# Optimization experiments

Measured on AMD Instinct MI355X. Metric: run time of the kernel, lower is better.

The kernel has to match this reference:

```python
import jax, jax.numpy as jnp
import numpy as np

DIM = 1024
HEADS = 16
HEAD_DIM = DIM // HEADS
SCALE = 1.0 / float(np.sqrt(HEAD_DIM))


def complex_linear(x, w_r, w_i, b_r, b_i):
    # x: (..., in, 2) with trailing real/imag channel
    xr, xi = x[..., 0], x[..., 1]
    lin_rr = xr @ w_r.T + b_r
    lin_ii = xi @ w_i.T + b_i
    lin_ri = xr @ w_i.T + b_i
    lin_ir = xi @ w_r.T + b_r
    out_r = lin_rr - lin_ii
    out_i = lin_ri + lin_ir
    return jnp.stack([out_r, out_i], axis=-1)


def setup_inputs() -> dict:
    key = jax.random.key(0)
    ks = jax.random.split(key, 9)
    B, N = 2, 2048
    s_in = 1.0 / np.sqrt(DIM)
    inp = {
        "x": jax.random.normal(ks[0], (B, N, DIM, 2), dtype=jnp.float32),
        "wqkv_r": jax.random.uniform(ks[1], (3 * DIM, DIM), jnp.float32, -s_in, s_in),
        "wqkv_i": jax.random.uniform(ks[2], (3 * DIM, DIM), jnp.float32, -s_in, s_in),
        "bqkv_r": jax.random.uniform(ks[3], (3 * DIM,), jnp.float32, -s_in, s_in),
        "bqkv_i": jax.random.uniform(ks[4], (3 * DIM,), jnp.float32, -s_in, s_in),
        "wo_r": jax.random.uniform(ks[5], (DIM, DIM), jnp.float32, -s_in, s_in),
        "wo_i": jax.random.uniform(ks[6], (DIM, DIM), jnp.float32, -s_in, s_in),
        "bo_r": jax.random.uniform(ks[7], (DIM,), jnp.float32, -s_in, s_in),
        "bo_i": jax.random.uniform(ks[8], (DIM,), jnp.float32, -s_in, s_in),
    }
    return inp


def reference(x, wqkv_r, wqkv_i, bqkv_r, bqkv_i, wo_r, wo_i, bo_r, bo_i):
    B, N, C, _ = x.shape
    qkv = complex_linear(x, wqkv_r, wqkv_i, bqkv_r, bqkv_i)  # (B,N,3C,2)
    q, k, v = jnp.split(qkv, 3, axis=-2)
    q = q.reshape(B, N, HEADS, HEAD_DIM, 2)
    k = k.reshape(B, N, HEADS, HEAD_DIM, 2)
    v = v.reshape(B, N, HEADS, HEAD_DIM, 2)
    # contract over head_dim AND complex channel: Re(q . conj(k))
    attn = jnp.einsum('bnhdc,bmhdc->bhnm', q, k) * SCALE
    attn = jax.nn.softmax(attn, axis=-1)
    out = jnp.einsum('bhnm,bmhdc->bnhdc', attn, v).reshape(B, N, C, 2)
    return complex_linear(out, wo_r, wo_i, bo_r, bo_i)
```

## Files before the change

### kernel.cpp

```cpp
#include <hip/hip_runtime.h>

using f16 = _Float16;
typedef f16 f16x8 __attribute__((ext_vector_type(8)));
typedef f16 f16x4 __attribute__((ext_vector_type(4)));
typedef float f32x4 __attribute__((ext_vector_type(4)));

#define TOKENS 4096
#define KD 2048
#define NQ 6144
#define QKW 4128
#define VTS 2064

__device__ __forceinline__ void gload_lds16(const void* g, void* l) {
  __builtin_amdgcn_global_load_lds(
      (__attribute__((address_space(1))) void*)(unsigned long long)g,
      (__attribute__((address_space(3))) void*)l, 16, 0, 0);
}

__global__ __launch_bounds__(256) void cast_x_kernel(const float* __restrict__ x,
                                                     f16* __restrict__ X, int n8) {
  int i = blockIdx.x * 256 + threadIdx.x;
  if (i >= n8) return;
  const float4* p = (const float4*)x + (size_t)i * 2;
  float4 a = p[0], b = p[1];
  f16x8 v = {(f16)a.x, (f16)a.y, (f16)a.z, (f16)a.w,
             (f16)b.x, (f16)b.y, (f16)b.z, (f16)b.w};
  *(f16x8*)(X + (size_t)i * 8) = v;
}

__global__ __launch_bounds__(256) void pack_wqkv_kernel(const float* __restrict__ wr,
    const float* __restrict__ wi, const float* __restrict__ br, const float* __restrict__ bi,
    f16* __restrict__ Wp, float* __restrict__ biasq) {
  int idx = blockIdx.x * 256 + threadIdx.x;
  if (idx >= NQ * 256) return;
  int j = idx >> 8, kc = idx & 255;
  int which = j >> 11, rem = j & 2047;
  int h = rem >> 7, t = rem & 127, d = t >> 1, c = t & 1;
  int o = which * 1024 + h * 64 + d;
  const float4 wr4 = *(const float4*)(wr + (size_t)o * 1024 + kc * 4);
  const float4 wi4 = *(const float4*)(wi + (size_t)o * 1024 + kc * 4);
  f16x8 v;
  const float wrs[4] = {wr4.x, wr4.y, wr4.z, wr4.w};
  const float wis[4] = {wi4.x, wi4.y, wi4.z, wi4.w};
  #pragma unroll
  for (int tt = 0; tt < 4; ++tt) {
    v[2 * tt]     = (f16)((c == 0) ? wrs[tt] : wis[tt]);
    v[2 * tt + 1] = (f16)((c == 0) ? -wis[tt] : wrs[tt]);
  }
  *(f16x8*)(Wp + (size_t)j * KD + kc * 8) = v;
  if (kc == 0) biasq[j] = (c == 0) ? (br[o] - bi[o]) : (br[o] + bi[o]);
}

__global__ __launch_bounds__(256) void pack_wo_kernel(const float* __restrict__ wr,
    const float* __restrict__ wi, const float* __restrict__ br, const float* __restrict__ bi,
    f16* __restrict__ Wp, float* __restrict__ biaso) {
  int idx = blockIdx.x * 256 + threadIdx.x;
  if (idx >= KD * 256) return;
  int j = idx >> 8, kc = idx & 255;
  int jo = j >> 1, c = j & 1;
  const float4 wr4 = *(const float4*)(wr + (size_t)jo * 1024 + kc * 4);
  const float4 wi4 = *(const float4*)(wi + (size_t)jo * 1024 + kc * 4);
  f16x8 v;
  const float wrs[4] = {wr4.x, wr4.y, wr4.z, wr4.w};
  const float wis[4] = {wi4.x, wi4.y, wi4.z, wi4.w};
  #pragma unroll
  for (int tt = 0; tt < 4; ++tt) {
    v[2 * tt]     = (f16)((c == 0) ? wrs[tt] : wis[tt]);
    v[2 * tt + 1] = (f16)((c == 0) ? -wis[tt] : wrs[tt]);
  }
  *(f16x8*)(Wp + (size_t)j * KD + kc * 8) = v;
  if (kc == 0) biaso[j] = (c == 0) ? (br[jo] - bi[jo]) : (br[jo] + bi[jo]);
}

template<bool QKV, int NTN>
__global__ __launch_bounds__(256, 3) void gemm_v5(const f16* __restrict__ A,
    const f16* __restrict__ B, const float* __restrict__ bias,
    f16* __restrict__ qkout, f16* __restrict__ vt, float* __restrict__ fout) {
  __shared__ __align__(16) f16 lA[128 * 64];
  __shared__ __align__(16) f16 lB[128 * 64];

  const int tid = threadIdx.x;
  const int wave = tid >> 6, lane = tid & 63;
  const int lo = lane & 15, hi = lane >> 4;
  const int wm = wave >> 1, wn = wave & 1;

  const int nwg = gridDim.x, cpx = nwg / 8;
  const int bid = blockIdx.x;
  const int wg = (bid & 7) * cpx + (bid >> 3);
  const int tm = wg / NTN, tn = wg % NTN;
  const int m0 = tm * 128, n0 = tn * 128;

  const f16* gA = A + (size_t)m0 * KD;
  const f16* gB = B + (size_t)n0 * KD;

  auto stage = [&](f16* ldsX, const f16* g) {
    #pragma unroll
    for (int is = 0; is < 4; ++is) {
      const int L = is * 256 + tid;
      const int row = L >> 3, cp = L & 7;
      gload_lds16(g + (size_t)row * KD + ((cp ^ (row & 7)) * 8),
                  ldsX + (size_t)(is * 256 + wave * 64) * 8);
    }
  };
  auto readA = [&](f16x8* dst, int kk) {
    #pragma unroll
    for (int i = 0; i < 4; ++i) {
      const int row = wm * 64 + i * 16 + lo;
      const int ch = (kk * 4 + hi) ^ (row & 7);
      dst[i] = *(const f16x8*)&lA[row * 64 + ch * 8];
    }
  };
  auto readB = [&](f16x8* dst, int kk) {
    #pragma unroll
    for (int i = 0; i < 4; ++i) {
      const int row = wn * 64 + i * 16 + lo;
      const int ch = (kk * 4 + hi) ^ (row & 7);
      dst[i] = *(const f16x8*)&lB[row * 64 + ch * 8];
    }
  };

  f32x4 acc[4][4] = {};

  for (int kt = 0; kt < KD; kt += 64) {
    __syncthreads();
    stage(lA, gA + kt);
    stage(lB, gB + kt);
    __syncthreads();
    f16x8 a[4], b[4];
    readA(a, 0); readB(b, 0);
    #pragma unroll
    for (int mi = 0; mi < 4; ++mi)
      #pragma unroll
      for (int ni = 0; ni < 4; ++ni)
        acc[mi][ni] = __builtin_amdgcn_mfma_f32_16x16x32_f16(a[mi], b[ni], acc[mi][ni], 0, 0, 0);
    readA(a, 1); readB(b, 1);
    #pragma unroll
    for (int mi = 0; mi < 4; ++mi)
      #pragma unroll
      for (int ni = 0; ni < 4; ++ni)
        acc[mi][ni] = __builtin_amdgcn_mfma_f32_16x16x32_f16(a[mi], b[ni], acc[mi][ni], 0, 0, 0);
  }

  #pragma unroll
  for (int mi = 0; mi < 4; ++mi) {
    #pragma unroll
    for (int ni = 0; ni < 4; ++ni) {
      const int colbase = n0 + wn * 64 + ni * 16;
      const int col = colbase + lo;
      const float bv = bias[col];
      const int rowb = m0 + wm * 64 + mi * 16 + hi * 4;
      if (QKV && colbase >= 4096) {
        const int dcol = col - 4096;
        const int hh = dcol >> 7, dd = dcol & 127;
        const int bb = rowb >> 11, tok = rowb & 2047;
        f16x4 pk;
        #pragma unroll
        for (int r = 0; r < 4; ++r) pk[r] = (f16)(acc[mi][ni][r] + bv);
        *(f16x4*)(vt + ((size_t)(bb * 16 + hh) * 128 + dd) * VTS + tok) = pk;
      } else if (QKV) {
        #pragma unroll
        for (int r = 0; r < 4; ++r)
          qkout[(size_t)(rowb + r) * QKW + col] = (f16)(acc[mi][ni][r] + bv);
      } else {
        #pragma unroll
        for (int r = 0; r < 4; ++r)
          fout[(size_t)(rowb + r) * KD + col] = acc[mi][ni][r] + bv;
      }
    }
  }
}

__global__ __launch_bounds__(256) void attn_kernel(const f16* __restrict__ qk,
                                                   const f16* __restrict__ vt,
                                                   f16* __restrict__ outp) {
  __shared__ __align__(16) f16 lds[2][8192];
  const int tid = threadIdx.x;
  const int wave = tid >> 6, lane = tid & 63;
  const int lo = lane & 15, hi = lane >> 4;

  const int flat = blockIdx.x;
  const int nf = (flat & 7) * 64 + (flat >> 3);
  const int by = nf >> 4, bx = nf & 15;
  const int b = by >> 4, h = by & 15;
  const int q0 = bx * 128 + wave * 32;

  const f16* Qb = qk + (size_t)b * 2048 * QKW + h * 128;
  const f16* Kb = Qb + 2048;
  const f16* Vtb = vt + (size_t)(b * 16 + h) * 128 * VTS;

  f16x8 qf[2][4];
  #pragma unroll
  for (int qb = 0; qb < 2; ++qb)
    #pragma unroll
    for (int c = 0; c < 4; ++c) {
      qf[qb][c] = *(const f16x8*)(Qb + (size_t)(q0 + qb * 16 + lo) * QKW + c * 32 + hi * 8);
      qf[qb][c] *= (f16)0.125f;
    }

  f32x4 o[2][8];
  #pragma unroll
  for (int qb = 0; qb < 2; ++qb)
    #pragma unroll
    for (int dc = 0; dc < 8; ++dc) o[qb][dc] = (f32x4){0.f, 0.f, 0.f, 0.f};
  float m_run[2] = {-INFINITY, -INFINITY};
  float l_run[2] = {0.f, 0.f};

  const int cl0 = wave * 64 + lane;

  auto STAGE = [&](int buf, int t) {
    #pragma unroll
    for (int rnd = 0; rnd < 2; ++rnd) {
      const int cl = rnd * 256 + cl0;
      const int row = cl >> 4;
      const int gch = (cl & 15) ^ (row & 7);
      gload_lds16(Kb + (size_t)(t + row) * QKW + gch * 8,
                  &lds[buf][(size_t)(rnd * 256 + wave * 64) * 8]);
    }
    #pragma unroll
    for (int rnd = 0; rnd < 2; ++rnd) {
      const int cl = rnd * 256 + cl0;
      const int d = cl >> 2;
      const int gch = (cl & 3) ^ ((d >> 1) & 3);
      gload_lds16(Vtb + (size_t)d * VTS + t + gch * 8,
                  &lds[buf][4096 + (size_t)(rnd * 256 + wave * 64) * 8]);
    }
  };

  STAGE(0, 0);
  int cur = 0;

  for (int it = 0; it < 64; ++it) {
    __syncthreads();
    if (it + 1 < 64) STAGE(cur ^ 1, (it + 1) * 32);

    const f16* ldsK = lds[cur];
    const f16* ldsV = lds[cur] + 4096;

    f16x8 kf[2][4];
    #pragma unroll
    for (int tt = 0; tt < 2; ++tt)
      #pragma unroll
      for (int c = 0; c < 4; ++c) {
        const int row = tt * 16 + lo;
        const int ch = (c * 4 + hi) ^ (row & 7);
        kf[tt][c] = *(const f16x8*)&ldsK[row * 128 + ch * 8];
      }

    f16x4 pf[2][2];
    #pragma unroll
    for (int qb = 0; qb < 2; ++qb) {
      f32x4 s0 = {0.f, 0.f, 0.f, 0.f}, s1 = {0.f, 0.f, 0.f, 0.f};
      #pragma unroll
      for (int c = 0; c < 4; ++c) {
        s0 = __builtin_amdgcn_mfma_f32_16x16x32_f16(kf[0][c], qf[qb][c], s0, 0, 0, 0);
        s1 = __builtin_amdgcn_mfma_f32_16x16x32_f16(kf[1][c], qf[qb][c], s1, 0, 0, 0);
      }

      float pm = fmaxf(fmaxf(fmaxf(s0[0], s0[1]), fmaxf(s0[2], s0[3])),
                       fmaxf(fmaxf(s1[0], s1[1]), fmaxf(s1[2], s1[3])));
      pm = fmaxf(pm, __shfl_xor(pm, 16));
      pm = fmaxf(pm, __shfl_xor(pm, 32));

      if (!__all(pm - m_run[qb] <= 8.f)) {
        const float corr = __expf(m_run[qb] - pm);
        m_run[qb] = pm;
        float co[4];
        #pragma unroll
        for (int r = 0; r < 4; ++r) co[r] = __shfl(corr, hi * 4 + r);
        #pragma unroll
        for (int dc = 0; dc < 8; ++dc)
          #pragma unroll
          for (int r = 0; r < 4; ++r) o[qb][dc][r] *= co[r];
        l_run[qb] *= corr;
      }

      float psum = 0.f;
      #pragma unroll
      for (int r = 0; r < 4; ++r) {
        const float p0 = __expf(s0[r] - m_run[qb]);
        const float p1 = __expf(s1[r] - m_run[qb]);
        psum += p0 + p1;
        pf[qb][0][r] = (f16)p0;
        pf[qb][1][r] = (f16)p1;
      }
      psum += __shfl_xor(psum, 16);
      psum += __shfl_xor(psum, 32);
      l_run[qb] += psum;
    }

    #pragma unroll
    for (int dc = 0; dc < 8; ++dc) {
      const int d = dc * 16 + lo;
      f16x4 vf[2];
      #pragma unroll
      for (int tt = 0; tt < 2; ++tt) {
        const int ch = (tt * 2 + (hi >> 1)) ^ ((d >> 1) & 3);
        vf[tt] = *(const f16x4*)&ldsV[d * 32 + ch * 8 + (hi & 1) * 4];
      }
      o[0][dc] = __builtin_amdgcn_mfma_f32_16x16x16f16(pf[0][0], vf[0], o[0][dc], 0, 0, 0);
      o[0][dc] = __builtin_amdgcn_mfma_f32_16x16x16f16(pf[0][1], vf[1], o[0][dc], 0, 0, 0);
      o[1][dc] = __builtin_amdgcn_mfma_f32_16x16x16f16(pf[1][0], vf[0], o[1][dc], 0, 0, 0);
      o[1][dc] = __builtin_amdgcn_mfma_f32_16x16x16f16(pf[1][1], vf[1], o[1][dc], 0, 0, 0);
    }

    cur ^= 1;
  }

  #pragma unroll
  for (int qb = 0; qb < 2; ++qb) {
    float inv[4];
    #pragma unroll
    for (int r = 0; r < 4; ++r) inv[r] = 1.f / __shfl(l_run[qb], hi * 4 + r);
    const int tok0 = b * 2048 + q0 + qb * 16;
    #pragma unroll
    for (int dc = 0; dc < 8; ++dc)
      #pragma unroll
      for (int r = 0; r < 4; ++r)
        outp[(size_t)(tok0 + hi * 4 + r) * KD + h * 128 + dc * 16 + lo] =
            (f16)(o[qb][dc][r] * inv[r]);
  }
}

extern "C" void kernel_launch(void* const* d_in, const int* in_sizes, int n_in,
                              void* d_out, int out_size, void* d_ws, size_t ws_size,
                              hipStream_t stream) {
  const float* x      = (const float*)d_in[0];
  const float* wqkv_r = (const float*)d_in[1];
  const float* wqkv_i = (const float*)d_in[2];
  const float* bqkv_r = (const float*)d_in[3];
  const float* bqkv_i = (const float*)d_in[4];
  const float* wo_r   = (const float*)d_in[5];
  const float* wo_i   = (const float*)d_in[6];
  const float* bo_r   = (const float*)d_in[7];
  const float* bo_i   = (const float*)d_in[8];
  float* out = (float*)d_out;
  char* ws = (char*)d_ws;

  f16*   Wqkv_p = (f16*)(ws + 0);
  f16*   Wo_p   = (f16*)(ws + 25165824);
  float* biasq  = (float*)(ws + 33554432);
  float* biaso  = (float*)(ws + 33579008);
  f16*   qkQK   = (f16*)(ws + 33587200);
  f16*   Vt     = (f16*)(ws + 67403776);
  f16*   Xh     = (f16*)(ws + 84312064);
  f16*   attn16 = Xh;

  cast_x_kernel<<<(TOKENS * KD / 8) / 256, 256, 0, stream>>>(x, Xh, TOKENS * KD / 8);
  pack_wqkv_kernel<<<(NQ * 256) / 256, 256, 0, stream>>>(wqkv_r, wqkv_i, bqkv_r, bqkv_i,
                                                         Wqkv_p, biasq);
  pack_wo_kernel<<<(KD * 256) / 256, 256, 0, stream>>>(wo_r, wo_i, bo_r, bo_i, Wo_p, biaso);

  gemm_v5<true, 48><<<1536, 256, 0, stream>>>(Xh, Wqkv_p, biasq, qkQK, Vt, nullptr);
  attn_kernel<<<512, 256, 0, stream>>>(qkQK, Vt, attn16);
  gemm_v5<false, 16><<<512, 256, 0, stream>>>(attn16, Wo_p, biaso, nullptr, nullptr, out);
}
```

Before: 317.7 us.

## Double attention KV tile to 64 keys, defer row-sum reduction, add MFMA priority

Each attention iteration now stages 64 keys instead of 32 into larger double-buffered LDS tiles. This halves the loop trip count and the number of barriers, and uses a new V-transpose swizzle sized for the wider tile. The per-iteration cross-lane reduction of the softmax denominator moves to a single reduction after the loop, and s_setprio wraps the MFMA blocks. In exchange, LDS use doubles to 64KB per block and more registers are live for the score tiles, which may reduce occupancy.

```diff
diff --git a/kernel.cpp b/kernel.cpp
--- a/kernel.cpp
+++ b/kernel.cpp
@@ -173,7 +173,7 @@
 __global__ __launch_bounds__(256) void attn_kernel(const f16* __restrict__ qk,
                                                    const f16* __restrict__ vt,
                                                    f16* __restrict__ outp) {
-  __shared__ __align__(16) f16 lds[2][8192];
+  __shared__ __align__(16) f16 lds[2][16384];
   const int tid = threadIdx.x;
   const int wave = tid >> 6, lane = tid & 63;
   const int lo = lane & 15, hi = lane >> 4;
@@ -205,59 +205,64 @@
   float m_run[2] = {-INFINITY, -INFINITY};
   float l_run[2] = {0.f, 0.f};
 
-  const int cl0 = wave * 64 + lane;
-
   auto STAGE = [&](int buf, int t) {
     #pragma unroll
-    for (int rnd = 0; rnd < 2; ++rnd) {
-      const int cl = rnd * 256 + cl0;
+    for (int rnd = 0; rnd < 4; ++rnd) {
+      const int cl = rnd * 256 + wave * 64 + lane;
       const int row = cl >> 4;
       const int gch = (cl & 15) ^ (row & 7);
       gload_lds16(Kb + (size_t)(t + row) * QKW + gch * 8,
                   &lds[buf][(size_t)(rnd * 256 + wave * 64) * 8]);
     }
     #pragma unroll
-    for (int rnd = 0; rnd < 2; ++rnd) {
-      const int cl = rnd * 256 + cl0;
-      const int d = cl >> 2;
-      const int gch = (cl & 3) ^ ((d >> 1) & 3);
+    for (int rnd = 0; rnd < 4; ++rnd) {
+      const int cl = rnd * 256 + wave * 64 + lane;
+      const int d = cl >> 3;
+      const int gch = (cl & 7) ^ (d & 7);
       gload_lds16(Vtb + (size_t)d * VTS + t + gch * 8,
-                  &lds[buf][4096 + (size_t)(rnd * 256 + wave * 64) * 8]);
+                  &lds[buf][8192 + (size_t)(rnd * 256 + wave * 64) * 8]);
     }
   };
 
   STAGE(0, 0);
   int cur = 0;
 
-  for (int it = 0; it < 64; ++it) {
+  for (int it = 0; it < 32; ++it) {
     __syncthreads();
-    if (it + 1 < 64) STAGE(cur ^ 1, (it + 1) * 32);
+    if (it + 1 < 32) STAGE(cur ^ 1, (it + 1) * 64);
 
     const f16* ldsK = lds[cur];
-    const f16* ldsV = lds[cur] + 4096;
-
-    f16x8 kf[2][4];
-    #pragma unroll
-    for (int tt = 0; tt < 2; ++tt)
+    const f16* ldsV = lds[cur] + 8192;
+
+    f32x4 s[2][4];
+    #pragma unroll
+    for (int tt = 0; tt < 4; ++tt) {
+      f16x8 kf[4];
       #pragma unroll
       for (int c = 0; c < 4; ++c) {
         const int row = tt * 16 + lo;
         const int ch = (c * 4 + hi) ^ (row & 7);
-        kf[tt][c] = *(const f16x8*)&ldsK[row * 128 + ch * 8];
-      }
-
-    f16x4 pf[2][2];
+        kf[c] = *(const f16x8*)&ldsK[row * 128 + ch * 8];
+      }
+      s[0][tt] = (f32x4){0.f, 0.f, 0.f, 0.f};
+      s[1][tt] = (f32x4){0.f, 0.f, 0.f, 0.f};
+      __builtin_amdgcn_s_setprio(1);
+      #pragma unroll
+      for (int c = 0; c < 4; ++c) {
+        s[0][tt] = __builtin_amdgcn_mfma_f32_16x16x32_f16(kf[c], qf[0][c], s[0][tt], 0, 0, 0);
+        s[1][tt] = __builtin_amdgcn_mfma_f32_16x16x32_f16(kf[c], qf[1][c], s[1][tt], 0, 0, 0);
+      }
+      __builtin_amdgcn_s_setprio(0);
+    }
+
+    f16x4 pf[2][4];
     #pragma unroll
     for (int qb = 0; qb < 2; ++qb) {
-      f32x4 s0 = {0.f, 0.f, 0.f, 0.f}, s1 = {0.f, 0.f, 0.f, 0.f};
-      #pragma unroll
-      for (int c = 0; c < 4; ++c) {
-        s0 = __builtin_amdgcn_mfma_f32_16x16x32_f16(kf[0][c], qf[qb][c], s0, 0, 0, 0);
-        s1 = __builtin_amdgcn_mfma_f32_16x16x32_f16(kf[1][c], qf[qb][c], s1, 0, 0, 0);
-      }
-
-      float pm = fmaxf(fmaxf(fmaxf(s0[0], s0[1]), fmaxf(s0[2], s0[3])),
-                       fmaxf(fmaxf(s1[0], s1[1]), fmaxf(s1[2], s1[3])));
+      float pm = -INFINITY;
+      #pragma unroll
+      for (int tt = 0; tt < 4; ++tt)
+        #pragma unroll
+        for (int r = 0; r < 4; ++r) pm = fmaxf(pm, s[qb][tt][r]);
       pm = fmaxf(pm, __shfl_xor(pm, 16));
       pm = fmaxf(pm, __shfl_xor(pm, 32));
 
@@ -276,31 +281,32 @@
 
       float psum = 0.f;
       #pragma unroll
-      for (int r = 0; r < 4; ++r) {
-        const float p0 = __expf(s0[r] - m_run[qb]);
-        const float p1 = __expf(s1[r] - m_run[qb]);
-        psum += p0 + p1;
-        pf[qb][0][r] = (f16)p0;
-        pf[qb][1][r] = (f16)p1;
-      }
-      psum += __shfl_xor(psum, 16);
-      psum += __shfl_xor(psum, 32);
+      for (int tt = 0; tt < 4; ++tt)
+        #pragma unroll
+        for (int r = 0; r < 4; ++r) {
+          const float p = __expf(s[qb][tt][r] - m_run[qb]);
+          psum += p;
+          pf[qb][tt][r] = (f16)p;
+        }
       l_run[qb] += psum;
     }
 
     #pragma unroll
     for (int dc = 0; dc < 8; ++dc) {
       const int d = dc * 16 + lo;
-      f16x4 vf[2];
-      #pragma unroll
-      for (int tt = 0; tt < 2; ++tt) {
-        const int ch = (tt * 2 + (hi >> 1)) ^ ((d >> 1) & 3);
-        vf[tt] = *(const f16x4*)&ldsV[d * 32 + ch * 8 + (hi & 1) * 4];
-      }
-      o[0][dc] = __builtin_amdgcn_mfma_f32_16x16x16f16(pf[0][0], vf[0], o[0][dc], 0, 0, 0);
-      o[0][dc] = __builtin_amdgcn_mfma_f32_16x16x16f16(pf[0][1], vf[1], o[0][dc], 0, 0, 0);
-      o[1][dc] = __builtin_amdgcn_mfma_f32_16x16x16f16(pf[1][0], vf[0], o[1][dc], 0, 0, 0);
-      o[1][dc] = __builtin_amdgcn_mfma_f32_16x16x16f16(pf[1][1], vf[1], o[1][dc], 0, 0, 0);
+      f16x4 vf[4];
+      #pragma unroll
+      for (int tt = 0; tt < 4; ++tt) {
+        const int ch = (tt * 2 + (hi >> 1)) ^ (d & 7);
+        vf[tt] = *(const f16x4*)&ldsV[d * 64 + ch * 8 + (hi & 1) * 4];
+      }
+      __builtin_amdgcn_s_setprio(1);
+      #pragma unroll
+      for (int tt = 0; tt < 4; ++tt) {
+        o[0][dc] = __builtin_amdgcn_mfma_f32_16x16x16f16(pf[0][tt], vf[tt], o[0][dc], 0, 0, 0);
+        o[1][dc] = __builtin_amdgcn_mfma_f32_16x16x16f16(pf[1][tt], vf[tt], o[1][dc], 0, 0, 0);
+      }
+      __builtin_amdgcn_s_setprio(0);
     }
 
     cur ^= 1;
@@ -308,6 +314,8 @@
 
   #pragma unroll
   for (int qb = 0; qb < 2; ++qb) {
+    l_run[qb] += __shfl_xor(l_run[qb], 16);
+    l_run[qb] += __shfl_xor(l_run[qb], 32);
     float inv[4];
     #pragma unroll
     for (int r = 0; r < 4; ++r) inv[r] = 1.f / __shfl(l_run[qb], hi * 4 + r);
```

Result: slower. 325.5 us (+2.4%).

## Use exp2 softmax with lazy rescale, deferred row-sum reduction and MFMA priority

Applied to the files above, without the earlier changes.

Folds log2(e) into the Q scale so probabilities use exp2 directly. The running max now starts at zero and is raised only when a wave sees growth above a threshold, and exponentials are computed before the max reduction. The per-iteration cross-lane reduction of the row sum is moved to the epilogue, and s_setprio wraps the MFMA blocks to favour matrix issue. The risk is fp16 overflow of probabilities when scores exceed the threshold before any rescale.

```diff
diff --git a/kernel.cpp b/kernel.cpp
--- a/kernel.cpp
+++ b/kernel.cpp
@@ -194,7 +194,7 @@
     #pragma unroll
     for (int c = 0; c < 4; ++c) {
       qf[qb][c] = *(const f16x8*)(Qb + (size_t)(q0 + qb * 16 + lo) * QKW + c * 32 + hi * 8);
-      qf[qb][c] *= (f16)0.125f;
+      qf[qb][c] *= (f16)0.18033688f;
     }
 
   f32x4 o[2][8];
@@ -202,15 +202,13 @@
   for (int qb = 0; qb < 2; ++qb)
     #pragma unroll
     for (int dc = 0; dc < 8; ++dc) o[qb][dc] = (f32x4){0.f, 0.f, 0.f, 0.f};
-  float m_run[2] = {-INFINITY, -INFINITY};
+  float m_run[2] = {0.f, 0.f};
   float l_run[2] = {0.f, 0.f};
 
-  const int cl0 = wave * 64 + lane;
-
   auto STAGE = [&](int buf, int t) {
     #pragma unroll
     for (int rnd = 0; rnd < 2; ++rnd) {
-      const int cl = rnd * 256 + cl0;
+      const int cl = rnd * 256 + wave * 64 + lane;
       const int row = cl >> 4;
       const int gch = (cl & 15) ^ (row & 7);
       gload_lds16(Kb + (size_t)(t + row) * QKW + gch * 8,
@@ -218,7 +216,7 @@
     }
     #pragma unroll
     for (int rnd = 0; rnd < 2; ++rnd) {
-      const int cl = rnd * 256 + cl0;
+      const int cl = rnd * 256 + wave * 64 + lane;
       const int d = cl >> 2;
       const int gch = (cl & 3) ^ ((d >> 1) & 3);
       gload_lds16(Vtb + (size_t)d * VTS + t + gch * 8,
@@ -250,10 +248,19 @@
     #pragma unroll
     for (int qb = 0; qb < 2; ++qb) {
       f32x4 s0 = {0.f, 0.f, 0.f, 0.f}, s1 = {0.f, 0.f, 0.f, 0.f};
+      __builtin_amdgcn_s_setprio(1);
       #pragma unroll
       for (int c = 0; c < 4; ++c) {
         s0 = __builtin_amdgcn_mfma_f32_16x16x32_f16(kf[0][c], qf[qb][c], s0, 0, 0, 0);
         s1 = __builtin_amdgcn_mfma_f32_16x16x32_f16(kf[1][c], qf[qb][c], s1, 0, 0, 0);
+      }
+      __builtin_amdgcn_s_setprio(0);
+
+      float p0[4], p1[4];
+      #pragma unroll
+      for (int r = 0; r < 4; ++r) {
+        p0[r] = __builtin_exp2f(s0[r] - m_run[qb]);
+        p1[r] = __builtin_exp2f(s1[r] - m_run[qb]);
       }
 
       float pm = fmaxf(fmaxf(fmaxf(s0[0], s0[1]), fmaxf(s0[2], s0[3])),
@@ -261,9 +268,13 @@
       pm = fmaxf(pm, __shfl_xor(pm, 16));
       pm = fmaxf(pm, __shfl_xor(pm, 32));
 
-      if (!__all(pm - m_run[qb] <= 8.f)) {
-        const float corr = __expf(m_run[qb] - pm);
-        m_run[qb] = pm;
+      if (__any(pm - m_run[qb] > 11.f)) {
+        const float mn = fmaxf(m_run[qb], pm);
+        const float corr = __builtin_exp2f(m_run[qb] - mn);
+        m_run[qb] = mn;
+        #pragma unroll
+        for (int r = 0; r < 4; ++r) { p0[r] *= corr; p1[r] *= corr; }
+        l_run[qb] *= corr;
         float co[4];
         #pragma unroll
         for (int r = 0; r < 4; ++r) co[r] = __shfl(corr, hi * 4 + r);
@@ -271,20 +282,15 @@
         for (int dc = 0; dc < 8; ++dc)
           #pragma unroll
           for (int r = 0; r < 4; ++r) o[qb][dc][r] *= co[r];
-        l_run[qb] *= corr;
       }
 
       float psum = 0.f;
       #pragma unroll
       for (int r = 0; r < 4; ++r) {
-        const float p0 = __expf(s0[r] - m_run[qb]);
-        const float p1 = __expf(s1[r] - m_run[qb]);
-        psum += p0 + p1;
-        pf[qb][0][r] = (f16)p0;
-        pf[qb][1][r] = (f16)p1;
-      }
-      psum += __shfl_xor(psum, 16);
-      psum += __shfl_xor(psum, 32);
+        psum += p0[r] + p1[r];
+        pf[qb][0][r] = (f16)p0[r];
+        pf[qb][1][r] = (f16)p1[r];
+      }
       l_run[qb] += psum;
     }
 
@@ -297,10 +303,12 @@
         const int ch = (tt * 2 + (hi >> 1)) ^ ((d >> 1) & 3);
         vf[tt] = *(const f16x4*)&ldsV[d * 32 + ch * 8 + (hi & 1) * 4];
       }
+      __builtin_amdgcn_s_setprio(1);
       o[0][dc] = __builtin_amdgcn_mfma_f32_16x16x16f16(pf[0][0], vf[0], o[0][dc], 0, 0, 0);
       o[0][dc] = __builtin_amdgcn_mfma_f32_16x16x16f16(pf[0][1], vf[1], o[0][dc], 0, 0, 0);
       o[1][dc] = __builtin_amdgcn_mfma_f32_16x16x16f16(pf[1][0], vf[0], o[1][dc], 0, 0, 0);
       o[1][dc] = __builtin_amdgcn_mfma_f32_16x16x16f16(pf[1][1], vf[1], o[1][dc], 0, 0, 0);
+      __builtin_amdgcn_s_setprio(0);
     }
 
     cur ^= 1;
@@ -308,6 +316,8 @@
 
   #pragma unroll
   for (int qb = 0; qb < 2; ++qb) {
+    l_run[qb] += __shfl_xor(l_run[qb], 16);
+    l_run[qb] += __shfl_xor(l_run[qb], 32);
     float inv[4];
     #pragma unroll
     for (int r = 0; r < 4; ++r) inv[r] = 1.f / __shfl(l_run[qb], hi * 4 + r);
```

After: 365.7 us. +15.1%, slower.

## Halve attention query tile per block to double grid size

Applied to the files above, without the earlier changes.

The attention kernel now gives each wave 16 query rows instead of 32, so each block covers 64 queries and the grid grows from 512 to 1024 blocks. This is meant to fill the 256 CUs more evenly and cut register pressure, which may allow higher occupancy. In exchange, K/V tiles are staged into LDS twice as often across the whole grid, lowering reuse of each loaded tile and raising total LDS and L2 traffic.

```diff
diff --git a/kernel.cpp b/kernel.cpp
--- a/kernel.cpp
+++ b/kernel.cpp
@@ -179,38 +179,32 @@
   const int lo = lane & 15, hi = lane >> 4;
 
   const int flat = blockIdx.x;
-  const int nf = (flat & 7) * 64 + (flat >> 3);
-  const int by = nf >> 4, bx = nf & 15;
+  const int nf = (flat & 7) * 128 + (flat >> 3);
+  const int by = nf >> 5, bx = nf & 31;
   const int b = by >> 4, h = by & 15;
-  const int q0 = bx * 128 + wave * 32;
+  const int q0 = bx * 64 + wave * 16;
 
   const f16* Qb = qk + (size_t)b * 2048 * QKW + h * 128;
   const f16* Kb = Qb + 2048;
   const f16* Vtb = vt + (size_t)(b * 16 + h) * 128 * VTS;
 
-  f16x8 qf[2][4];
-  #pragma unroll
-  for (int qb = 0; qb < 2; ++qb)
-    #pragma unroll
-    for (int c = 0; c < 4; ++c) {
-      qf[qb][c] = *(const f16x8*)(Qb + (size_t)(q0 + qb * 16 + lo) * QKW + c * 32 + hi * 8);
-      qf[qb][c] *= (f16)0.125f;
-    }
-
-  f32x4 o[2][8];
-  #pragma unroll
-  for (int qb = 0; qb < 2; ++qb)
-    #pragma unroll
-    for (int dc = 0; dc < 8; ++dc) o[qb][dc] = (f32x4){0.f, 0.f, 0.f, 0.f};
-  float m_run[2] = {-INFINITY, -INFINITY};
-  float l_run[2] = {0.f, 0.f};
-
-  const int cl0 = wave * 64 + lane;
+  f16x8 qf[4];
+  #pragma unroll
+  for (int c = 0; c < 4; ++c) {
+    qf[c] = *(const f16x8*)(Qb + (size_t)(q0 + lo) * QKW + c * 32 + hi * 8);
+    qf[c] *= (f16)0.125f;
+  }
+
+  f32x4 o[8];
+  #pragma unroll
+  for (int dc = 0; dc < 8; ++dc) o[dc] = (f32x4){0.f, 0.f, 0.f, 0.f};
+  float m_run = -INFINITY;
+  float l_run = 0.f;
 
   auto STAGE = [&](int buf, int t) {
     #pragma unroll
     for (int rnd = 0; rnd < 2; ++rnd) {
-      const int cl = rnd * 256 + cl0;
+      const int cl = rnd * 256 + wave * 64 + lane;
       const int row = cl >> 4;
       const int gch = (cl & 15) ^ (row & 7);
       gload_lds16(Kb + (size_t)(t + row) * QKW + gch * 8,
@@ -218,7 +212,7 @@
     }
     #pragma unroll
     for (int rnd = 0; rnd < 2; ++rnd) {
-      const int cl = rnd * 256 + cl0;
+      const int cl = rnd * 256 + wave * 64 + lane;
       const int d = cl >> 2;
       const int gch = (cl & 3) ^ ((d >> 1) & 3);
       gload_lds16(Vtb + (size_t)d * VTS + t + gch * 8,
@@ -246,47 +240,44 @@
         kf[tt][c] = *(const f16x8*)&ldsK[row * 128 + ch * 8];
       }
 
-    f16x4 pf[2][2];
-    #pragma unroll
-    for (int qb = 0; qb < 2; ++qb) {
-      f32x4 s0 = {0.f, 0.f, 0.f, 0.f}, s1 = {0.f, 0.f, 0.f, 0.f};
-      #pragma unroll
-      for (int c = 0; c < 4; ++c) {
-        s0 = __builtin_amdgcn_mfma_f32_16x16x32_f16(kf[0][c], qf[qb][c], s0, 0, 0, 0);
-        s1 = __builtin_amdgcn_mfma_f32_16x16x32_f16(kf[1][c], qf[qb][c], s1, 0, 0, 0);
-      }
-
-      float pm = fmaxf(fmaxf(fmaxf(s0[0], s0[1]), fmaxf(s0[2], s0[3])),
-                       fmaxf(fmaxf(s1[0], s1[1]), fmaxf(s1[2], s1[3])));
-      pm = fmaxf(pm, __shfl_xor(pm, 16));
-      pm = fmaxf(pm, __shfl_xor(pm, 32));
-
-      if (!__all(pm - m_run[qb] <= 8.f)) {
-        const float corr = __expf(m_run[qb] - pm);
-        m_run[qb] = pm;
-        float co[4];
+    f32x4 s0 = {0.f, 0.f, 0.f, 0.f}, s1 = {0.f, 0.f, 0.f, 0.f};
+    #pragma unroll
+    for (int c = 0; c < 4; ++c) {
+      s0 = __builtin_amdgcn_mfma_f32_16x16x32_f16(kf[0][c], qf[c], s0, 0, 0, 0);
+      s1 = __builtin_amdgcn_mfma_f32_16x16x32_f16(kf[1][c], qf[c], s1, 0, 0, 0);
+    }
+
+    float pm = fmaxf(fmaxf(fmaxf(s0[0], s0[1]), fmaxf(s0[2], s0[3])),
+                     fmaxf(fmaxf(s1[0], s1[1]), fmaxf(s1[2], s1[3])));
+    pm = fmaxf(pm, __shfl_xor(pm, 16));
+    pm = fmaxf(pm, __shfl_xor(pm, 32));
+
+    if (!__all(pm - m_run <= 8.f)) {
+      const float corr = __expf(m_run - pm);
+      m_run = pm;
+      float co[4];
+      #pragma unroll
+      for (int r = 0; r < 4; ++r) co[r] = __shfl(corr, hi * 4 + r);
+      #pragma unroll
+      for (int dc = 0; dc < 8; ++dc)
         #pragma unroll
-        for (int r = 0; r < 4; ++r) co[r] = __shfl(corr, hi * 4 + r);
-        #pragma unroll
-        for (int dc = 0; dc < 8; ++dc)
-          #pragma unroll
-          for (int r = 0; r < 4; ++r) o[qb][dc][r] *= co[r];
-        l_run[qb] *= corr;
-      }
-
-      float psum = 0.f;
-      #pragma unroll
-      for (int r = 0; r < 4; ++r) {
-        const float p0 = __expf(s0[r] - m_run[qb]);
-        const float p1 = __expf(s1[r] - m_run[qb]);
-        psum += p0 + p1;
-        pf[qb][0][r] = (f16)p0;
-        pf[qb][1][r] = (f16)p1;
-      }
-      psum += __shfl_xor(psum, 16);
-      psum += __shfl_xor(psum, 32);
-      l_run[qb] += psum;
-    }
+        for (int r = 0; r < 4; ++r) o[dc][r] *= co[r];
+      l_run *= corr;
+    }
+
+    f16x4 pf0, pf1;
+    float psum = 0.f;
+    #pragma unroll
+    for (int r = 0; r < 4; ++r) {
+      const float p0 = __expf(s0[r] - m_run);
+      const float p1 = __expf(s1[r] - m_run);
+      psum += p0 + p1;
+      pf0[r] = (f16)p0;
+      pf1[r] = (f16)p1;
+    }
+    psum += __shfl_xor(psum, 16);
+    psum += __shfl_xor(psum, 32);
+    l_run += psum;
 
     #pragma unroll
     for (int dc = 0; dc < 8; ++dc) {
@@ -297,28 +288,23 @@
         const int ch = (tt * 2 + (hi >> 1)) ^ ((d >> 1) & 3);
         vf[tt] = *(const f16x4*)&ldsV[d * 32 + ch * 8 + (hi & 1) * 4];
       }
-      o[0][dc] = __builtin_amdgcn_mfma_f32_16x16x16f16(pf[0][0], vf[0], o[0][dc], 0, 0, 0);
-      o[0][dc] = __builtin_amdgcn_mfma_f32_16x16x16f16(pf[0][1], vf[1], o[0][dc], 0, 0, 0);
-      o[1][dc] = __builtin_amdgcn_mfma_f32_16x16x16f16(pf[1][0], vf[0], o[1][dc], 0, 0, 0);
-      o[1][dc] = __builtin_amdgcn_mfma_f32_16x16x16f16(pf[1][1], vf[1], o[1][dc], 0, 0, 0);
+      o[dc] = __builtin_amdgcn_mfma_f32_16x16x16f16(pf0, vf[0], o[dc], 0, 0, 0);
+      o[dc] = __builtin_amdgcn_mfma_f32_16x16x16f16(pf1, vf[1], o[dc], 0, 0, 0);
     }
 
     cur ^= 1;
   }
 
-  #pragma unroll
-  for (int qb = 0; qb < 2; ++qb) {
-    float inv[4];
-    #pragma unroll
-    for (int r = 0; r < 4; ++r) inv[r] = 1.f / __shfl(l_run[qb], hi * 4 + r);
-    const int tok0 = b * 2048 + q0 + qb * 16;
-    #pragma unroll
-    for (int dc = 0; dc < 8; ++dc)
-      #pragma unroll
-      for (int r = 0; r < 4; ++r)
-        outp[(size_t)(tok0 + hi * 4 + r) * KD + h * 128 + dc * 16 + lo] =
-            (f16)(o[qb][dc][r] * inv[r]);
-  }
+  float inv[4];
+  #pragma unroll
+  for (int r = 0; r < 4; ++r) inv[r] = 1.f / __shfl(l_run, hi * 4 + r);
+  const int tok0 = b * 2048 + q0;
+  #pragma unroll
+  for (int dc = 0; dc < 8; ++dc)
+    #pragma unroll
+    for (int r = 0; r < 4; ++r)
+      outp[(size_t)(tok0 + hi * 4 + r) * KD + h * 128 + dc * 16 + lo] =
+          (f16)(o[dc][r] * inv[r]);
 }
 
 extern "C" void kernel_launch(void* const* d_in, const int* in_sizes, int n_in,
@@ -351,6 +337,6 @@
   pack_wo_kernel<<<(KD * 256) / 256, 256, 0, stream>>>(wo_r, wo_i, bo_r, bo_i, Wo_p, biaso);
 
   gemm_v5<true, 48><<<1536, 256, 0, stream>>>(Xh, Wqkv_p, biasq, qkQK, Vt, nullptr);
-  attn_kernel<<<512, 256, 0, stream>>>(qkQK, Vt, attn16);
+  attn_kernel<<<1024, 256, 0, stream>>>(qkQK, Vt, attn16);
   gemm_v5<false, 16><<<512, 256, 0, stream>>>(attn16, Wo_p, biaso, nullptr, nullptr, out);
 }
```

Result: slower. 351.0 us (+10.5%).
